# Performance work log

Hardware: AMD Instinct MI355X
Metric: run time of the kernel (lower is better)

## Reference

```python
import jax, jax.numpy as jnp
import numpy as np

N_NODES = 100000
N_EDGES = 1600000
IN_CH = 128
OUT_CH = 128
N_REL = 64
N_BASES = 8


def setup_inputs() -> dict:
    key = jax.random.key(0)
    k = jax.random.split(key, 7)
    x = jax.random.normal(k[0], (N_NODES, IN_CH), dtype=jnp.float32)
    src = jax.random.randint(k[1], (N_EDGES,), 0, N_NODES, dtype=jnp.int32)
    rel = jax.random.randint(k[2], (N_EDGES,), 0, N_REL, dtype=jnp.int32)
    dst = jax.random.randint(k[3], (N_EDGES,), 0, N_NODES, dtype=jnp.int32)
    edge_triples = jnp.stack([src, rel, dst], axis=1)  # [E, 3] (src, rel, dst)
    # xavier-uniform-ish scales
    basis = jax.random.normal(k[4], (N_BASES, IN_CH, OUT_CH), dtype=jnp.float32) * (2.0 / (IN_CH + OUT_CH)) ** 0.5
    att = jax.random.normal(k[5], (N_REL, N_BASES), dtype=jnp.float32) * (2.0 / (N_REL + N_BASES)) ** 0.5
    root_w = jax.random.normal(k[6], (IN_CH, OUT_CH), dtype=jnp.float32) * (1.0 / IN_CH) ** 0.5
    root_b = jnp.zeros((OUT_CH,), dtype=jnp.float32)
    return {"x": x, "edge_triples": edge_triples, "num_nodes": N_NODES,
            "basis": basis, "att": att, "root_w": root_w, "root_b": root_b}


def reference(x, edge_triples, num_nodes, basis, att, root_w, root_b):
    src = edge_triples[:, 0]
    rel = edge_triples[:, 1]
    dst = edge_triples[:, 2]
    att_e = att[rel]  # [E, B]
    n_bases = basis.shape[0]
    e = src.shape[0]
    out_ch = basis.shape[2]
    # messages[e] = x[src[e]] @ (sum_b att[rel[e], b] * basis[b])
    # computed as sum_b att_e[:, b] * (x @ basis[b])[src] to avoid the huge
    # per-edge [E, in, out] weight gather the torch code materializes.
    msgs = jnp.zeros((e, out_ch), dtype=x.dtype)
    for b in range(n_bases):  # small fixed loop over bases
        yb = x @ basis[b]  # [N, out]
        msgs = msgs + att_e[:, b:b + 1] * yb[src]
    # degree normalization (mean aggregation over incoming edges)
    deg = jax.ops.segment_sum(jnp.ones((e,), dtype=x.dtype), dst, num_segments=num_nodes)
    deg_inv = jnp.where(deg > 0, 1.0 / deg, 0.0)
    msgs = msgs * deg_inv[dst][:, None]
    agg = jax.ops.segment_sum(msgs, dst, num_segments=num_nodes)  # [N, out]
    return agg + x @ root_w + root_b
```

## Files before the change

kernel.cpp:

```cpp
#include <hip/hip_runtime.h>

#define NCH 128
#define NREL 64
#define NBP 1024
#define ESB 4096
#define CAPF 3072
#define CAPH 2048
#define KTOT 1152
#define KST 36
#define ZROW 2304

typedef __attribute__((ext_vector_type(8))) short bf16x8;
typedef __attribute__((ext_vector_type(4))) float f32x4;

__device__ __forceinline__ unsigned short f2bf(float f) {
    unsigned u = __float_as_uint(f);
    return (unsigned short)((u + 0x7fffu + ((u >> 16) & 1u)) >> 16);
}
__device__ __forceinline__ unsigned pack2bf(float a, float b) {
    return (unsigned)f2bf(a) | ((unsigned)f2bf(b) << 16);
}

__global__ __launch_bounds__(256) void k_prep(const float* __restrict__ x,
                                              unsigned short* __restrict__ xsw,
                                              int N) {
    int idx = blockIdx.x * 256 + threadIdx.x;
    if (idx >= N * 16) return;
    int n = idx >> 4, l15 = idx & 15;
    const float* xr = x + (size_t)n * NCH + l15;
    bf16x8 p;
#pragma unroll
    for (int nt = 0; nt < 8; ++nt) p[nt] = (short)f2bf(xr[nt * 16]);
    *(bf16x8*)(xsw + (size_t)n * NCH + l15 * 8) = p;
}

__global__ __launch_bounds__(256) void k_buildB(const float* __restrict__ basis,
                                                const float* __restrict__ att,
                                                const float* __restrict__ rw,
                                                unsigned short* __restrict__ attB2,
                                                unsigned short* __restrict__ basisP) {
    int idx = blockIdx.x * 256 + threadIdx.x;
    if (idx < 2080) {
        int rr = idx >> 5, p = (idx >> 4) & 1, m = idx & 15;
        attB2[idx] = (rr < NREL && (m >> 3) == p) ? f2bf(att[rr * 8 + (m & 7)])
                                                  : (unsigned short)0;
    }
    if (idx >= 128 * KTOT) return;
    int j = idx & 7, lg = (idx >> 3) & 3, oc = (idx >> 5) & 127, kk = idx >> 12;
    int k = kk * 32 + lg * 8 + j;
    float v;
    if (k < 1024) {
        int b = k & 7, ch = k >> 3;
        v = basis[(size_t)b * NCH * NCH + (size_t)ch * NCH + oc];
    } else {
        int kp = k - 1024;
        int ic = ((kp & 7) << 4) | (kp >> 3);
        v = rw[(size_t)ic * NCH + oc];
    }
    basisP[idx] = f2bf(v);
}

__global__ __launch_bounds__(256) void k_count(const int* __restrict__ trip, int E, int NB,
                                               int* __restrict__ cntB) {
    __shared__ int hb[NBP];
    int t = threadIdx.x;
    for (int i = t; i < NB; i += 256) hb[i] = 0;
    __syncthreads();
    int base = blockIdx.x * ESB;
#pragma unroll
    for (int i = 0; i < ESB / 256; ++i) {
        int e = base + i * 256 + t;
        if (e < E) atomicAdd(&hb[trip[3 * e + 2] >> 7], 1);
    }
    __syncthreads();
    for (int i = t; i < NB; i += 256) cntB[(size_t)blockIdx.x * NB + i] = hb[i];
}

__global__ __launch_bounds__(1024) void k_scanB(int* __restrict__ cntB, int GB, int NB,
                                                int* __restrict__ bhist) {
    __shared__ int sc[1024];
    int t = threadIdx.x, b = blockIdx.x;
    int v = (t < GB) ? cntB[(size_t)t * NB + b] : 0;
    sc[t] = v;
    __syncthreads();
    for (int off = 1; off < 1024; off <<= 1) {
        int a = (t >= off) ? sc[t - off] : 0;
        __syncthreads();
        sc[t] += a;
        __syncthreads();
    }
    if (t < GB) cntB[(size_t)t * NB + b] = sc[t] - v;
    if (t == GB - 1) bhist[b] = sc[t];
}

__global__ __launch_bounds__(1024) void k_offsets(const int* __restrict__ bhist, int NB,
                                                  int* __restrict__ bucketoff) {
    __shared__ int sc[1024];
    int t = threadIdx.x;
    int d = (t < NB) ? bhist[t] : 0;
    sc[t] = d;
    __syncthreads();
    for (int off = 1; off < 1024; off <<= 1) {
        int a = (t >= off) ? sc[t - off] : 0;
        __syncthreads();
        sc[t] += a;
        __syncthreads();
    }
    if (t < NB) bucketoff[t] = sc[t] - d;
    if (t == NB - 1) bucketoff[NB] = sc[t];
}

__global__ __launch_bounds__(256) void k_scatter(const int* __restrict__ trip, int E, int NB,
                                                 const int* __restrict__ cntB,
                                                 const int* __restrict__ bucketoff,
                                                 unsigned* __restrict__ packed) {
    __shared__ int cb[NBP], lbase[NBP], delta[NBP];
    __shared__ int ssc[256];
    __shared__ unsigned lpk[ESB];
    __shared__ unsigned short lb[ESB];
    int t = threadIdx.x, blk = blockIdx.x;
    for (int i = t; i < NB; i += 256) cb[i] = 0;
    __syncthreads();
    int base = blk * ESB;
    int total = min(ESB, E - base);

    unsigned pk[ESB / 256];
    int rk[ESB / 256];
    unsigned short bk[ESB / 256];
#pragma unroll
    for (int i = 0; i < ESB / 256; ++i) {
        int e = base + i * 256 + t;
        pk[i] = 0; rk[i] = 0; bk[i] = 0;
        if (e < E) {
            int src = trip[3 * e], rel = trip[3 * e + 1], dst = trip[3 * e + 2];
            int bkt = dst >> 7;
            bk[i] = (unsigned short)bkt;
            pk[i] = ((unsigned)(dst & 127) << 23) | ((unsigned)rel << 17) | (unsigned)src;
            rk[i] = atomicAdd(&cb[bkt], 1);
        }
    }
    __syncthreads();
    int ch = (NB + 255) >> 8;
    int mysum = 0;
    for (int i = 0; i < ch; ++i) {
        int idx = t * ch + i;
        if (idx < NB) mysum += cb[idx];
    }
    ssc[t] = mysum;
    __syncthreads();
    for (int off = 1; off < 256; off <<= 1) {
        int a = (t >= off) ? ssc[t - off] : 0;
        __syncthreads();
        ssc[t] += a;
        __syncthreads();
    }
    int run = ssc[t] - mysum;
    for (int i = 0; i < ch; ++i) {
        int idx = t * ch + i;
        if (idx < NB) { lbase[idx] = run; run += cb[idx]; }
    }
    __syncthreads();
    for (int i = t; i < NB; i += 256)
        delta[i] = bucketoff[i] + cntB[(size_t)blk * NB + i] - lbase[i];
    __syncthreads();
#pragma unroll
    for (int i = 0; i < ESB / 256; ++i) {
        int e = base + i * 256 + t;
        if (e < E) {
            int j = lbase[bk[i]] + rk[i];
            lpk[j] = pk[i];
            lb[j] = bk[i];
        }
    }
    __syncthreads();
    for (int j = t; j < total; j += 256)
        packed[delta[lb[j]] + j] = lpk[j];
}

__global__ __launch_bounds__(256) void k_sortbkt(const unsigned* __restrict__ packed,
                                                 const int* __restrict__ bucketoff,
                                                 unsigned* __restrict__ sortedG,
                                                 int* __restrict__ dstoffG) {
    __shared__ int h[128], hs[128];
    int t = threadIdx.x, b = blockIdx.x;
    if (t < 128) h[t] = 0;
    __syncthreads();
    int s0 = bucketoff[b], s1 = bucketoff[b + 1];
    int cnt = min(s1 - s0, CAPF);

    unsigned pk[CAPF / 256];
    int rk[CAPF / 256];
#pragma unroll
    for (int i = 0; i < CAPF / 256; ++i) {
        int j = i * 256 + t;
        pk[i] = 0; rk[i] = 0;
        if (j < cnt) {
            unsigned p = packed[s0 + j];
            pk[i] = p;
            rk[i] = atomicAdd(&h[p >> 23], 1);
        }
    }
    __syncthreads();
    if (t < 128) hs[t] = h[t];
    __syncthreads();
    for (int off = 1; off < 128; off <<= 1) {
        int a = (t < 128 && t >= off) ? hs[t - off] : 0;
        __syncthreads();
        if (t < 128) hs[t] += a;
        __syncthreads();
    }
    if (t < 128) dstoffG[b * 129 + t] = hs[t] - h[t];
    if (t == 0) dstoffG[b * 129 + 128] = cnt;
#pragma unroll
    for (int i = 0; i < CAPF / 256; ++i) {
        int j = i * 256 + t;
        if (j < cnt) {
            int d = pk[i] >> 23;
            sortedG[s0 + hs[d] - h[d] + rk[i]] = pk[i];
        }
    }
}

__global__ __launch_bounds__(512, 4) void k_fused(const unsigned* __restrict__ x32,
                                                  const char* __restrict__ xswb,
                                                  const unsigned* __restrict__ sortedG,
                                                  const int* __restrict__ bucketoff,
                                                  const int* __restrict__ dstoffG,
                                                  const unsigned short* __restrict__ attBg,
                                                  const unsigned short* __restrict__ basisP,
                                                  const float* __restrict__ rb,
                                                  float* __restrict__ out, int N) {
    __shared__ bf16x8 ztV[16 * (ZROW / 16)];
    __shared__ unsigned sortedE[CAPH];
    __shared__ unsigned short attl[2080];
    __shared__ int doffsL[65];
    __shared__ int nextD;
    char* zt = (char*)ztV;

    int t = threadIdx.x;
    int bucket = blockIdx.x >> 1, half = blockIdx.x & 1;
    int w = t >> 6, lane = t & 63, lr = lane & 15, lg = lane >> 4;
    int l15 = lane & 15;
    int nb0 = bucket * 128 + half * 64;

    for (int i = t; i < 2080; i += 512) attl[i] = attBg[i];
    int rawIdx = bucket * 129 + half * 64;
    int rawBase = dstoffG[rawIdx];
    int cnt = min(dstoffG[rawIdx + 64] - rawBase, CAPH);
    if (t < 65) doffsL[t] = min(dstoffG[rawIdx + t] - rawBase, CAPH);
    if (t == 0) nextD = 0;
    int sG0 = bucketoff[bucket] + rawBase;
    for (int j = t; j < cnt; j += 512) {
        unsigned p = sortedG[sG0 + j];
        sortedE[j] = (((p >> 17) & 63u) << 26) | ((p & 0x1FFFFu) << 8) | ((p >> 23) & 1u);
    }
    __syncthreads();

    const char* xl = xswb + (l15 << 4);

    for (int r = 0; r < 4; ++r) {
        int rEnd = r * 8 + 8;

        for (;;) {
            int my = 0x7FFFFFFF;
            if (lane == 0) my = atomicAdd(&nextD, 1);
            my = __shfl(my, 0, 64);
            if (my >= rEnd) break;
            int d0 = my * 2, d1 = d0 + 1;
            int eBeg = doffsL[d0], eMid = doffsL[d0 + 1], eEnd = doffsL[d0 + 2];
            int cnt0 = eMid - eBeg, cnt1 = eEnd - eMid;
            int n0 = nb0 + d0, n1 = nb0 + d1;
            unsigned xv0 = (n0 < N) ? x32[(size_t)n0 * 64 + lane] : 0u;
            unsigned xv1 = (n1 < N) ? x32[(size_t)n1 * 64 + lane] : 0u;

            float inv0 = (cnt0 > 0) ? 1.f / (float)cnt0 : 0.f;
            float inv1 = (cnt1 > 0) ? 1.f / (float)cnt1 : 0.f;
            int pr = lg >> 1;
            float invM = pr ? inv1 : inv0;
            int dz = (pr ? d1 : d0) & 15;
            char* zrowM = zt + dz * ZROW;
            int swM = dz & 7;
            int b0 = (lg & 1) << 2;
            int last = eEnd - 1;

#pragma unroll 1
            for (int hp = 0; hp < 2; ++hp) {
                f32x4 acc[4];
#pragma unroll
                for (int q = 0; q < 4; ++q) acc[q] = (f32x4){0.f, 0.f, 0.f, 0.f};

                for (int c0 = eBeg; c0 < eEnd; c0 += 32) {
                    int kb = c0 + (lg << 3);
                    bf16x8 aF;
                    uint2 lo[8];
#pragma unroll
                    for (int j = 0; j < 8; ++j) {
                        int e = kb + j;
                        unsigned ew = sortedE[min(e, last)];
                        int arow = (e < eEnd) ? (int)(((ew >> 26) << 5) | ((ew & 1u) << 4))
                                              : 2048;
                        aF[j] = (short)attl[arow + l15];
                        lo[j] = *(const uint2*)(xl + (ew & 0x03FFFF00u) + hp * 8);
                    }
#pragma unroll
                    for (int q = 0; q < 4; ++q) {
                        unsigned sel = (q & 1) ? 0x03020706u : 0x01000504u;
                        int h = q >> 1;
                        unsigned bw[4];
                        bw[0] = __builtin_amdgcn_perm(((const unsigned*)&lo[0])[h],
                                                      ((const unsigned*)&lo[1])[h], sel);
                        bw[1] = __builtin_amdgcn_perm(((const unsigned*)&lo[2])[h],
                                                      ((const unsigned*)&lo[3])[h], sel);
                        bw[2] = __builtin_amdgcn_perm(((const unsigned*)&lo[4])[h],
                                                      ((const unsigned*)&lo[5])[h], sel);
                        bw[3] = __builtin_amdgcn_perm(((const unsigned*)&lo[6])[h],
                                                      ((const unsigned*)&lo[7])[h], sel);
                        acc[q] = __builtin_amdgcn_mfma_f32_16x16x32_bf16(
                            aF, *(const bf16x8*)&bw[0], acc[q], 0, 0, 0);
                    }
                }
#pragma unroll
                for (int q = 0; q < 4; ++q) {
                    int chn = (hp * 4 + q) * 16 + l15;
                    uint2 v;
                    v.x = pack2bf(acc[q][0] * invM, acc[q][1] * invM);
                    v.y = pack2bf(acc[q][2] * invM, acc[q][3] * invM);
                    *(uint2*)(zrowM + ((chn ^ swM) << 4) + (b0 << 1)) = v;
                }
            }
            {
                int z0 = d0 & 15, z1 = d1 & 15;
                char* zr0 = zt + z0 * ZROW;
                char* zr1 = zt + z1 * ZROW;
                int u = 128 + (lane >> 2), sub = (lane & 3) << 2;
                *(unsigned*)(zr0 + (((u) ^ (z0 & 7)) << 4) + sub) = xv0;
                *(unsigned*)(zr1 + (((u) ^ (z1 & 7)) << 4) + sub) = xv1;
            }
        }
        __syncthreads();

        f32x4 accM = {0.f, 0.f, 0.f, 0.f};
        int ocr = w * 16 + lr;
        int swm = lr & 7;
#pragma unroll 6
        for (int kk = 0; kk < KST; ++kk) {
            bf16x8 a = *(const bf16x8*)(zt + lr * ZROW + ((((kk << 2) + lg) ^ swm) << 4));
            bf16x8 b0 = *(const bf16x8*)(basisP + ((((size_t)kk * 128 + ocr) * 4 + lg) << 3));
            accM = __builtin_amdgcn_mfma_f32_16x16x32_bf16(b0, a, accM, 0, 0, 0);
        }

        int n = nb0 + r * 16 + lr;
        if (n < N) {
            int oc0 = w * 16 + lg * 4;
            f32x4 bias = *(const f32x4*)(rb + oc0);
            *(f32x4*)(out + (size_t)n * NCH + oc0) = accM + bias;
        }
        if (t == 0) nextD = rEnd;
        __syncthreads();
    }
}

extern "C" void kernel_launch(void* const* d_in, const int* in_sizes, int n_in,
                              void* d_out, int out_size, void* d_ws, size_t ws_size,
                              hipStream_t stream) {
    const float* x = (const float*)d_in[0];
    const int* trip = (const int*)d_in[1];
    const float* basis = (const float*)d_in[3];
    const float* att = (const float*)d_in[4];
    const float* rw = (const float*)d_in[5];
    const float* rb = (const float*)d_in[6];
    float* out = (float*)d_out;

    int N = in_sizes[0] / NCH;
    int E = in_sizes[1] / 3;
    int NB = (N + 127) >> 7;
    int GB = (E + ESB - 1) / ESB;

    char* ws = (char*)d_ws;
    size_t off = 0;
    auto alloc = [&](size_t bts) { size_t o = off; off = (off + bts + 255) & ~(size_t)255; return o; };
    size_t oXbf    = alloc((size_t)N * NCH * 2);
    size_t oBasisP = alloc((size_t)128 * KTOT * 2);
    size_t oAttB   = alloc(2080 * 2);
    size_t oCntB   = alloc((size_t)GB * NB * 4);
    size_t oBhist  = alloc((NBP + 1) * 4);
    size_t oBktoff = alloc((NBP + 1) * 4);
    size_t oPacked = alloc((size_t)E * 4);
    size_t oSorted = alloc((size_t)E * 4);
    size_t oDoff   = alloc((size_t)NB * 129 * 4);
    (void)off; (void)ws_size;

    unsigned short* x_sw = (unsigned short*)(ws + oXbf);
    unsigned short* basisP = (unsigned short*)(ws + oBasisP);
    unsigned short* attB = (unsigned short*)(ws + oAttB);
    int* cntB = (int*)(ws + oCntB);
    int* bhist = (int*)(ws + oBhist);
    int* bucketoff = (int*)(ws + oBktoff);
    unsigned* packed = (unsigned*)(ws + oPacked);
    unsigned* sortedG = (unsigned*)(ws + oSorted);
    int* dstoffG = (int*)(ws + oDoff);

    k_prep<<<(N * 16 + 255) / 256, 256, 0, stream>>>(x, x_sw, N);
    k_buildB<<<(128 * KTOT + 255) / 256, 256, 0, stream>>>(basis, att, rw, attB, basisP);
    k_count<<<GB, 256, 0, stream>>>(trip, E, NB, cntB);
    k_scanB<<<NB, 1024, 0, stream>>>(cntB, GB, NB, bhist);
    k_offsets<<<1, 1024, 0, stream>>>(bhist, NB, bucketoff);
    k_scatter<<<GB, 256, 0, stream>>>(trip, E, NB, cntB, bucketoff, packed);
    k_sortbkt<<<NB, 256, 0, stream>>>(packed, bucketoff, sortedG, dstoffG);
    k_fused<<<NB * 2, 512, 0, stream>>>((const unsigned*)x_sw, (const char*)x_sw, sortedG,
                                        bucketoff, dstoffG, attB, basisP, rb, out, N);
}
```

Before: 255.1 us.

## Pad per-pair edge segments to 32 and precompute inverse degrees

The sort kernel now writes edges into fixed-capacity per-half-bucket slots, with each destination pair's segment padded to a multiple of 32 and filled with sentinel entries. Degree counts go out separately and the fused kernel precomputes inverse degrees in shared memory. The fused kernel's inner gather loop drops its per-edge bounds clamp and select: padding entries map to a zero attention row and node 0. In exchange, sortedG is filled with sentinels, the workspace grows, and pairs whose padded total exceeds CAPH silently drop edges.

```diff
diff --git a/kernel.cpp b/kernel.cpp
--- a/kernel.cpp
+++ b/kernel.cpp
@@ -5,7 +5,7 @@
 #define NBP 1024
 #define ESB 4096
 #define CAPF 3072
-#define CAPH 2048
+#define CAPH 2304
 #define KTOT 1152
 #define KST 36
 #define ZROW 2304
@@ -180,8 +180,10 @@
 __global__ __launch_bounds__(256) void k_sortbkt(const unsigned* __restrict__ packed,
                                                  const int* __restrict__ bucketoff,
                                                  unsigned* __restrict__ sortedG,
-                                                 int* __restrict__ dstoffG) {
-    __shared__ int h[128], hs[128];
+                                                 int* __restrict__ pairoffG,
+                                                 int* __restrict__ dstcntG) {
+    __shared__ int h[128];
+    __shared__ int ppo[2][33];
     int t = threadIdx.x, b = blockIdx.x;
     if (t < 128) h[t] = 0;
     __syncthreads();
@@ -201,22 +203,32 @@
         }
     }
     __syncthreads();
-    if (t < 128) hs[t] = h[t];
-    __syncthreads();
-    for (int off = 1; off < 128; off <<= 1) {
-        int a = (t < 128 && t >= off) ? hs[t - off] : 0;
-        __syncthreads();
-        if (t < 128) hs[t] += a;
-        __syncthreads();
-    }
-    if (t < 128) dstoffG[b * 129 + t] = hs[t] - h[t];
-    if (t == 0) dstoffG[b * 129 + 128] = cnt;
+    if (t < 2) {
+        int base2 = 0;
+        for (int pl = 0; pl < 32; ++pl) {
+            ppo[t][pl] = base2;
+            int pc = h[t * 64 + 2 * pl] + h[t * 64 + 2 * pl + 1];
+            int pad = ((pc + 31) >> 5) << 5;
+            base2 = min(base2 + pad, CAPH);
+        }
+        ppo[t][32] = base2;
+    }
+    for (int j = t; j < 2 * CAPH; j += 256)
+        sortedG[(size_t)b * 2 * CAPH + j] = 0x80000000u;
+    __syncthreads();
+    if (t < 128) dstcntG[b * 128 + t] = h[t];
+    if (t < 33) pairoffG[(b * 2 + 0) * 33 + t] = ppo[0][t];
+    else if (t < 66) pairoffG[(b * 2 + 1) * 33 + (t - 33)] = ppo[1][t - 33];
 #pragma unroll
     for (int i = 0; i < CAPF / 256; ++i) {
         int j = i * 256 + t;
         if (j < cnt) {
-            int d = pk[i] >> 23;
-            sortedG[s0 + hs[d] - h[d] + rk[i]] = pk[i];
+            unsigned p = pk[i];
+            int d = p >> 23;
+            int half = d >> 6, pl = (d & 63) >> 1;
+            int off = ppo[half][pl] + ((d & 1) ? h[d - 1] : 0) + rk[i];
+            if (off < ppo[half][pl + 1])
+                sortedG[(size_t)b * 2 * CAPH + half * CAPH + off] = p;
         }
     }
 }
@@ -224,8 +236,8 @@
 __global__ __launch_bounds__(512, 4) void k_fused(const unsigned* __restrict__ x32,
                                                   const char* __restrict__ xswb,
                                                   const unsigned* __restrict__ sortedG,
-                                                  const int* __restrict__ bucketoff,
-                                                  const int* __restrict__ dstoffG,
+                                                  const int* __restrict__ pairoffG,
+                                                  const int* __restrict__ dstcntG,
                                                   const unsigned short* __restrict__ attBg,
                                                   const unsigned short* __restrict__ basisP,
                                                   const float* __restrict__ rb,
@@ -233,7 +245,8 @@
     __shared__ bf16x8 ztV[16 * (ZROW / 16)];
     __shared__ unsigned sortedE[CAPH];
     __shared__ unsigned short attl[2080];
-    __shared__ int doffsL[65];
+    __shared__ int pairoffL[33];
+    __shared__ float invL[64];
     __shared__ int nextD;
     char* zt = (char*)ztV;
 
@@ -244,15 +257,20 @@
     int nb0 = bucket * 128 + half * 64;
 
     for (int i = t; i < 2080; i += 512) attl[i] = attBg[i];
-    int rawIdx = bucket * 129 + half * 64;
-    int rawBase = dstoffG[rawIdx];
-    int cnt = min(dstoffG[rawIdx + 64] - rawBase, CAPH);
-    if (t < 65) doffsL[t] = min(dstoffG[rawIdx + t] - rawBase, CAPH);
+    if (t < 33) pairoffL[t] = pairoffG[(bucket * 2 + half) * 33 + t];
+    if (t >= 64 && t < 128) {
+        int c = dstcntG[bucket * 128 + half * 64 + (t - 64)];
+        invL[t - 64] = c ? 1.f / (float)c : 0.f;
+    }
     if (t == 0) nextD = 0;
-    int sG0 = bucketoff[bucket] + rawBase;
-    for (int j = t; j < cnt; j += 512) {
-        unsigned p = sortedG[sG0 + j];
-        sortedE[j] = (((p >> 17) & 63u) << 26) | ((p & 0x1FFFFu) << 8) | ((p >> 23) & 1u);
+    int cntPad = pairoffG[(bucket * 2 + half) * 33 + 32];
+    size_t slotBase = (size_t)(bucket * 2 + half) * CAPH;
+    for (int j = t; j < cntPad; j += 512) {
+        unsigned p = sortedG[slotBase + j];
+        unsigned word;
+        if (p & 0x80000000u) word = (2048u << 20);
+        else word = (((p >> 17) & 63u) << 25) | (((p >> 23) & 1u) << 24) | (p & 0x1FFFFu);
+        sortedE[j] = word;
     }
     __syncthreads();
 
@@ -267,24 +285,21 @@
             my = __shfl(my, 0, 64);
             if (my >= rEnd) break;
             int d0 = my * 2, d1 = d0 + 1;
-            int eBeg = doffsL[d0], eMid = doffsL[d0 + 1], eEnd = doffsL[d0 + 2];
-            int cnt0 = eMid - eBeg, cnt1 = eEnd - eMid;
+            int eBeg = pairoffL[my], eEnd = pairoffL[my + 1];
             int n0 = nb0 + d0, n1 = nb0 + d1;
             unsigned xv0 = (n0 < N) ? x32[(size_t)n0 * 64 + lane] : 0u;
             unsigned xv1 = (n1 < N) ? x32[(size_t)n1 * 64 + lane] : 0u;
 
-            float inv0 = (cnt0 > 0) ? 1.f / (float)cnt0 : 0.f;
-            float inv1 = (cnt1 > 0) ? 1.f / (float)cnt1 : 0.f;
             int pr = lg >> 1;
-            float invM = pr ? inv1 : inv0;
+            float invM = pr ? invL[d1] : invL[d0];
             int dz = (pr ? d1 : d0) & 15;
             char* zrowM = zt + dz * ZROW;
             int swM = dz & 7;
             int b0 = (lg & 1) << 2;
-            int last = eEnd - 1;
 
 #pragma unroll 1
             for (int hp = 0; hp < 2; ++hp) {
+                const char* xh = xl + hp * 8;
                 f32x4 acc[4];
 #pragma unroll
                 for (int q = 0; q < 4; ++q) acc[q] = (f32x4){0.f, 0.f, 0.f, 0.f};
@@ -295,12 +310,9 @@
                     uint2 lo[8];
 #pragma unroll
                     for (int j = 0; j < 8; ++j) {
-                        int e = kb + j;
-                        unsigned ew = sortedE[min(e, last)];
-                        int arow = (e < eEnd) ? (int)(((ew >> 26) << 5) | ((ew & 1u) << 4))
-                                              : 2048;
-                        aF[j] = (short)attl[arow + l15];
-                        lo[j] = *(const uint2*)(xl + (ew & 0x03FFFF00u) + hp * 8);
+                        unsigned ew = sortedE[kb + j];
+                        aF[j] = (short)attl[(ew >> 20) + l15];
+                        lo[j] = *(const uint2*)(xh + ((ew & 0x1FFFFu) << 8));
                     }
 #pragma unroll
                     for (int q = 0; q < 4; ++q) {
@@ -386,8 +398,9 @@
     size_t oBhist  = alloc((NBP + 1) * 4);
     size_t oBktoff = alloc((NBP + 1) * 4);
     size_t oPacked = alloc((size_t)E * 4);
-    size_t oSorted = alloc((size_t)E * 4);
-    size_t oDoff   = alloc((size_t)NB * 129 * 4);
+    size_t oSorted = alloc((size_t)NB * 2 * CAPH * 4);
+    size_t oPairoff = alloc((size_t)NB * 2 * 33 * 4);
+    size_t oDstcnt = alloc((size_t)NB * 128 * 4);
     (void)off; (void)ws_size;
 
     unsigned short* x_sw = (unsigned short*)(ws + oXbf);
@@ -398,7 +411,8 @@
     int* bucketoff = (int*)(ws + oBktoff);
     unsigned* packed = (unsigned*)(ws + oPacked);
     unsigned* sortedG = (unsigned*)(ws + oSorted);
-    int* dstoffG = (int*)(ws + oDoff);
+    int* pairoffG = (int*)(ws + oPairoff);
+    int* dstcntG = (int*)(ws + oDstcnt);
 
     k_prep<<<(N * 16 + 255) / 256, 256, 0, stream>>>(x, x_sw, N);
     k_buildB<<<(128 * KTOT + 255) / 256, 256, 0, stream>>>(basis, att, rw, attB, basisP);
@@ -406,7 +420,7 @@
     k_scanB<<<NB, 1024, 0, stream>>>(cntB, GB, NB, bhist);
     k_offsets<<<1, 1024, 0, stream>>>(bhist, NB, bucketoff);
     k_scatter<<<GB, 256, 0, stream>>>(trip, E, NB, cntB, bucketoff, packed);
-    k_sortbkt<<<NB, 256, 0, stream>>>(packed, bucketoff, sortedG, dstoffG);
+    k_sortbkt<<<NB, 256, 0, stream>>>(packed, bucketoff, sortedG, pairoffG, dstcntG);
     k_fused<<<NB * 2, 512, 0, stream>>>((const unsigned*)x_sw, (const char*)x_sw, sortedG,
-                                        bucketoff, dstoffG, attB, basisP, rb, out, N);
-}
+                                        pairoffG, dstcntG, attB, basisP, rb, out, N);
+}
```

Result: no change. 252.1 us (-1.2%).
